# Performance work log

Measured on AMD Instinct MI355X. Metric: run time of the kernel, lower is better.

Reference implementation:

```python
import jax, jax.numpy as jnp
import numpy as np

D_MODEL = 1024
NUM_HEADS = 16
D_HEAD = D_MODEL // NUM_HEADS
EPS = 1e-06


def setup_inputs() -> dict:
    key = jax.random.key(0)
    ks = jax.random.split(key, 11)
    B, T = 16, 8192
    s = 1.0 / np.sqrt(D_MODEL)
    inp = {
        "query": jax.random.normal(ks[0], (B, 1, D_MODEL), jnp.float32),
        "key": jax.random.normal(ks[1], (B, T, D_MODEL), jnp.float32),
        "value": jax.random.normal(ks[2], (B, T, D_MODEL), jnp.float32),
        "Wq": jax.random.normal(ks[3], (D_MODEL, D_MODEL), jnp.float32) * s,
        "bq": jnp.zeros((D_MODEL,), jnp.float32),
        "Wk": jax.random.normal(ks[4], (D_MODEL, D_MODEL), jnp.float32) * s,
        "bk": jnp.zeros((D_MODEL,), jnp.float32),
        "Wv": jax.random.normal(ks[5], (D_MODEL, D_MODEL), jnp.float32) * s,
        "bv": jnp.zeros((D_MODEL,), jnp.float32),
        "Wo": jax.random.normal(ks[6], (D_MODEL, D_MODEL), jnp.float32) * s,
        "bo": jnp.zeros((D_MODEL,), jnp.float32),
    }
    return inp


def _feature_map(x):
    # ELU + 1 ensures positivity
    return jax.nn.elu(x) + 1.0


def reference(query, key, value, Wq, bq, Wk, bk, Wv, bv, Wo, bo):
    B, T, _ = key.shape
    H, dh = NUM_HEADS, D_HEAD
    # projections (torch Linear: x @ W^T + b)
    Q = (query @ Wq.T + bq).reshape(B, 1, H, dh).transpose(0, 2, 1, 3)  # [B,H,1,dh]
    K = (key @ Wk.T + bk).reshape(B, T, H, dh).transpose(0, 2, 1, 3)    # [B,H,T,dh]
    V = (value @ Wv.T + bv).reshape(B, T, H, dh).transpose(0, 2, 1, 3)  # [B,H,T,dh]
    Q = _feature_map(Q)
    K = _feature_map(K)
    # linear-attention accumulators
    KV = jnp.einsum("bhtd,bhte->bhde", K, V)        # [B,H,dh,dh]
    Z = K.sum(axis=2)                                  # [B,H,dh]
    num = jnp.einsum("bhqd,bhde->bhqe", Q, KV)       # [B,H,1,dh]
    den = jnp.einsum("bhqd,bhd->bhq", Q, Z)[..., None]  # [B,H,1,1]
    out = num / (den + EPS)
    out = out.transpose(0, 2, 1, 3).reshape(B, 1, D_MODEL)
    return out @ Wo.T + bo
```

## Files before the change

kernel.cpp:

```cpp
#include <hip/hip_runtime.h>


typedef __attribute__((ext_vector_type(8))) short  bf16x8;
typedef __attribute__((ext_vector_type(4))) short  bf16x4;
typedef __attribute__((ext_vector_type(4))) float  f32x4;

#define WS_QPHI 0u
#define WS_PRE  65536u
#define WS_S    131072u
#define WS_WKB  1179648u
#define WS_W    3276800u

__device__ __forceinline__ unsigned short f2bf(float f) {
  union { float f; unsigned u; } c; c.f = f;
  unsigned u = c.u;
  return (unsigned short)((u + 0x7fffu + ((u >> 16) & 1u)) >> 16);
}

__device__ __forceinline__ unsigned cvt_pk_bf16(float lo, float hi) {
  unsigned r;
  asm("v_cvt_pk_bf16_f32 %0, %1, %2" : "=v"(r) : "v"(lo), "v"(hi));
  return r;
}

__device__ __forceinline__ uint4 pack_bf16x8(f32x4 x, f32x4 y) {
  uint4 r;
  r.x = cvt_pk_bf16(x[0], x[1]); r.y = cvt_pk_bf16(x[2], x[3]);
  r.z = cvt_pk_bf16(y[0], y[1]); r.w = cvt_pk_bf16(y[2], y[3]);
  return r;
}

__device__ __forceinline__ void gload_lds16(const void* g, void* l) {
  __builtin_amdgcn_global_load_lds((const __attribute__((address_space(1))) void*)g,
                                   (__attribute__((address_space(3))) void*)l, 16, 0, 0);
}

__global__ void k_convert_wk(const float* __restrict__ Wk, unsigned short* __restrict__ Wkb) {
  int i = blockIdx.x * 256 + threadIdx.x;
  f32x4 v = ((const f32x4*)Wk)[i];
  bf16x4 o;
  o[0] = (short)f2bf(v[0]); o[1] = (short)f2bf(v[1]);
  o[2] = (short)f2bf(v[2]); o[3] = (short)f2bf(v[3]);
  ((bf16x4*)Wkb)[i] = o;
}

__global__ void k_qproj(const float* __restrict__ q, const float* __restrict__ Wq,
                        const float* __restrict__ bq, float* __restrict__ Qphi) {
  int b = blockIdx.x, h = blockIdx.y, d = threadIdx.x;
  const f32x4* qr = (const f32x4*)(q + b * 1024);
  const f32x4* wr = (const f32x4*)(Wq + (size_t)(h * 64 + d) * 1024);
  float s = bq[h * 64 + d];
  for (int i = 0; i < 256; ++i) {
    f32x4 a = qr[i], ww = wr[i];
    s += a[0]*ww[0] + a[1]*ww[1] + a[2]*ww[2] + a[3]*ww[3];
  }
  s = s > 0.f ? s + 1.f : __expf(s);
  Qphi[(b * 16 + h) * 64 + d] = s;
}

__global__ __launch_bounds__(512, 4)
void k_kproj(const float* __restrict__ key, const unsigned short* __restrict__ Wkb,
             const float* __restrict__ bk, const float* __restrict__ Qphi,
             float* __restrict__ w) {
  __shared__ __align__(16) unsigned short sA[2][128 * 40];
  __shared__ __align__(16) unsigned short sB[3][256 * 32];

  const int bid  = blockIdx.x + (blockIdx.y << 2);
  const int work = ((bid & 7) << 9) | (bid >> 3);
  const int np   = work & 3;
  const int mb   = work >> 2;
  const int b    = mb >> 6;
  const int mrow = (mb & 63) << 7;
  const int tid  = threadIdx.x;
  const int lane = tid & 63;
  const int wv   = tid >> 6;
  const int wr   = wv >> 2;
  const int wc   = wv & 3;
  const int n0   = np << 8;
  const int h    = (np << 2) | wc;
  const int l15  = lane & 15;
  const int lk   = (lane >> 4) << 3;

  const int ar = tid >> 2, aq = tid & 3;
  const float* Ab = key + ((size_t)((b << 13) + mrow + ar)) * 1024 + aq * 8;
  const int sAoff = ar * 40 + aq * 8;

  const int bsw = ((lane & 3) ^ ((lane >> 3) & 3)) << 3;
  const unsigned short* Bb = Wkb + ((size_t)(n0 + (wv << 5) + (lane >> 2))) * 1024 + bsw;
  const int fsw = (l15 >> 1) & 3;

  f32x4 acc[4][4];
  #pragma unroll
  for (int i = 0; i < 4; ++i)
    #pragma unroll
    for (int j = 0; j < 4; ++j) acc[i][j] = (f32x4)0.f;

  float qreg[4];
  #pragma unroll
  for (int ni = 0; ni < 4; ++ni)
    qreg[ni] = Qphi[((b << 4) + h) * 64 + ni * 16 + l15];

  f32x4 a0 = *(const f32x4*)(Ab);
  f32x4 a1 = *(const f32x4*)(Ab + 4);
  __builtin_amdgcn_sched_barrier(0);
  gload_lds16(Bb,                  &sB[0][wv * 1024]);
  gload_lds16(Bb + 16 * 1024,      &sB[0][wv * 1024 + 512]);
  gload_lds16(Bb + 32,             &sB[1][wv * 1024]);
  gload_lds16(Bb + 16 * 1024 + 32, &sB[1][wv * 1024 + 512]);
  __builtin_amdgcn_sched_barrier(0);
  *(uint4*)&sA[0][sAoff] = pack_bf16x8(a0, a1);
  asm volatile("s_waitcnt vmcnt(2) lgkmcnt(0)" ::: "memory");
  __builtin_amdgcn_s_barrier();
  __builtin_amdgcn_sched_barrier(0);

  #pragma unroll 1
  for (int t = 0; t < 32; ++t) {
    if (t < 31) {
      const float* An = Ab + (t + 1) * 32;
      a0 = *(const f32x4*)(An);
      a1 = *(const f32x4*)(An + 4);
    }
    __builtin_amdgcn_sched_barrier(0);
    if (t < 30) {
      const unsigned short* Bn = Bb + (t + 2) * 32;
      const int bn = (t + 2) % 3;
      gload_lds16(Bn,             &sB[bn][wv * 1024]);
      gload_lds16(Bn + 16 * 1024, &sB[bn][wv * 1024 + 512]);
    }
    __builtin_amdgcn_sched_barrier(0);
    {
      const unsigned short* pA = &sA[t & 1][0];
      const unsigned short* pB = &sB[t % 3][0];
      bf16x8 af[4], bfr[4];
      #pragma unroll
      for (int mi = 0; mi < 4; ++mi)
        af[mi] = *(const bf16x8*)&pA[((wr << 6) + mi * 16 + l15) * 40 + lk];
      #pragma unroll
      for (int ni = 0; ni < 4; ++ni)
        bfr[ni] = *(const bf16x8*)&pB[((wc << 6) + ni * 16 + l15) * 32
                                      + (((lane >> 4) ^ fsw) << 3)];
      #pragma unroll
      for (int mi = 0; mi < 4; ++mi)
        #pragma unroll
        for (int ni = 0; ni < 4; ++ni)
          acc[mi][ni] = __builtin_amdgcn_mfma_f32_16x16x32_bf16(af[mi], bfr[ni], acc[mi][ni], 0, 0, 0);
    }
    if (t < 31)
      *(uint4*)&sA[(t + 1) & 1][sAoff] = pack_bf16x8(a0, a1);
    if (t < 30)      asm volatile("s_waitcnt vmcnt(2) lgkmcnt(0)" ::: "memory");
    else if (t < 31) asm volatile("s_waitcnt vmcnt(0) lgkmcnt(0)" ::: "memory");
    if (t < 31) {
      __builtin_amdgcn_s_barrier();
      __builtin_amdgcn_sched_barrier(0);
    }
  }

  float bias[4];
  #pragma unroll
  for (int ni = 0; ni < 4; ++ni) bias[ni] = bk[n0 + (wc << 6) + ni * 16 + l15];

  #pragma unroll
  for (int mi = 0; mi < 4; ++mi) {
    float wa[4];
    #pragma unroll
    for (int r = 0; r < 4; ++r) {
      float s = 0.f;
      #pragma unroll
      for (int ni = 0; ni < 4; ++ni) {
        float x = acc[mi][ni][r] + bias[ni];
        x = x > 0.f ? x + 1.f : __expf(x);
        s += x * qreg[ni];
      }
      wa[r] = s;
    }
    #pragma unroll
    for (int m = 1; m < 16; m <<= 1)
      #pragma unroll
      for (int r = 0; r < 4; ++r) wa[r] += __shfl_xor(wa[r], m, 64);
    if (l15 == 0) {
      const int rg = lane >> 4;
      #pragma unroll
      for (int r = 0; r < 4; ++r) {
        int trow = mrow + (wr << 6) + mi * 16 + (rg << 2) + r;
        w[(((size_t)((b << 4) + h)) << 13) + trow] = wa[r];
      }
    }
  }
}

__global__ __launch_bounds__(256)
void k_sgemm(const float* __restrict__ value, const float* __restrict__ w,
             float* __restrict__ S) {
  __shared__ float wl[16 * 256];
  const int b = blockIdx.x, tc = blockIdx.y;
  const int t0 = tc << 8;
  const int tid = threadIdx.x;
  for (int i = tid; i < 16 * 256; i += 256)
    wl[i] = w[(((size_t)(b * 16 + (i >> 8))) << 13) + t0 + (i & 255)];
  __syncthreads();
  f32x4 acc[16];
  #pragma unroll
  for (int h = 0; h < 16; ++h) acc[h] = (f32x4)0.f;
  const f32x4* vb = (const f32x4*)(value + ((size_t)(b << 13) + t0) * 1024) + tid;
  #pragma unroll 4
  for (int t = 0; t < 256; ++t) {
    f32x4 x = vb[t << 8];
    #pragma unroll
    for (int h = 0; h < 16; ++h)
      acc[h] += x * wl[(h << 8) + t];
  }
  #pragma unroll
  for (int h = 0; h < 16; ++h) {
    float* sp = S + ((b << 4) + h) * 1024 + (tid << 2);
    atomicAdd(sp + 0, acc[h][0]); atomicAdd(sp + 1, acc[h][1]);
    atomicAdd(sp + 2, acc[h][2]); atomicAdd(sp + 3, acc[h][3]);
  }
}

__global__ __launch_bounds__(256)
void k_numden(const float* __restrict__ w, const float* __restrict__ S,
              const float* __restrict__ Wv, const float* __restrict__ bv,
              float* __restrict__ pre) {
  __shared__ float red[2][4][64];
  const int b = blockIdx.x, h = blockIdx.y;
  const int tid = threadIdx.x, e = tid & 63, part = tid >> 6;
  const float* wb = w + (((size_t)(b * 16 + h)) << 13);
  float dsum = 0.f;
  for (int i = part * 32; i < part * 32 + 32; ++i) dsum += wb[i * 64 + e];
  const f32x4* sr  = (const f32x4*)(S + (b * 16 + h) * 1024);
  const f32x4* wvr = (const f32x4*)(Wv + (size_t)(h * 64 + e) * 1024);
  float ns = 0.f;
  for (int i = part * 64; i < part * 64 + 64; ++i) {
    f32x4 a = sr[i], c = wvr[i];
    ns += a[0]*c[0] + a[1]*c[1] + a[2]*c[2] + a[3]*c[3];
  }
  red[0][part][e] = dsum; red[1][part][e] = ns;
  __syncthreads();
  if (part == 0) {
    float d = red[0][0][e] + red[0][1][e] + red[0][2][e] + red[0][3][e];
    float n = red[1][0][e] + red[1][1][e] + red[1][2][e] + red[1][3][e];
    #pragma unroll
    for (int m = 1; m < 64; m <<= 1) d += __shfl_xor(d, m, 64);
    n += d * bv[h * 64 + e];
    pre[b * 1024 + h * 64 + e] = n / (d + 1e-6f);
  }
}

__global__ __launch_bounds__(256)
void k_outproj(const float* __restrict__ pre, const float* __restrict__ Wo,
               const float* __restrict__ bo, float* __restrict__ out) {
  __shared__ float pl[1024];
  const int b = blockIdx.x, ch = blockIdx.y;
  const int tid = threadIdx.x, lane = tid & 63, wv = tid >> 6;
  for (int i = tid; i < 1024; i += 256) pl[i] = pre[b * 1024 + i];
  __syncthreads();
  for (int oi = 0; oi < 32; ++oi) {
    int o = (ch << 7) + (wv << 5) + oi;
    const f32x4* wrow = (const f32x4*)(Wo + (size_t)o * 1024);
    float s = 0.f;
    #pragma unroll
    for (int j = 0; j < 4; ++j) {
      f32x4 v = wrow[lane * 4 + j];
      f32x4 p = *(const f32x4*)&pl[(lane * 4 + j) * 4];
      s += v[0]*p[0] + v[1]*p[1] + v[2]*p[2] + v[3]*p[3];
    }
    #pragma unroll
    for (int m = 1; m < 64; m <<= 1) s += __shfl_xor(s, m, 64);
    if (lane == 0) out[b * 1024 + o] = s + bo[o];
  }
}

extern "C" void kernel_launch(void* const* d_in, const int* in_sizes, int n_in,
                              void* d_out, int out_size, void* d_ws, size_t ws_size,
                              hipStream_t stream) {
  const float* query = (const float*)d_in[0];
  const float* key   = (const float*)d_in[1];
  const float* value = (const float*)d_in[2];
  const float* Wq    = (const float*)d_in[3];
  const float* bq    = (const float*)d_in[4];
  const float* Wk    = (const float*)d_in[5];
  const float* bk    = (const float*)d_in[6];
  const float* Wv    = (const float*)d_in[7];
  const float* bv    = (const float*)d_in[8];
  const float* Wo    = (const float*)d_in[9];
  const float* bo    = (const float*)d_in[10];
  float* out = (float*)d_out;
  char* ws = (char*)d_ws;
  float*          Qphi = (float*)(ws + WS_QPHI);
  float*          pre  = (float*)(ws + WS_PRE);
  float*          S    = (float*)(ws + WS_S);
  unsigned short* Wkb  = (unsigned short*)(ws + WS_WKB);
  float*          w    = (float*)(ws + WS_W);

  hipMemsetAsync(S, 0, 16 * 16 * 1024 * sizeof(float), stream);
  k_convert_wk<<<1024, 256, 0, stream>>>(Wk, Wkb);
  k_qproj<<<dim3(16, 16), 64, 0, stream>>>(query, Wq, bq, Qphi);
  k_kproj<<<dim3(4, 1024), 512, 0, stream>>>(key, Wkb, bk, Qphi, w);
  k_sgemm<<<dim3(16, 32), 256, 0, stream>>>(value, w, S);
  k_numden<<<dim3(16, 16), 256, 0, stream>>>(w, S, Wv, bv, pre);
  k_outproj<<<dim3(16, 8), 256, 0, stream>>>(pre, Wo, bo, out);
}
```

Measured before the change: 653.1 us.

## Enlarge kproj GEMM tile to 256x256 with split-phase MFMA pipeline

The key-projection GEMM tile grows from 128x256 to 256x256 rows per block, with each wave now covering 128 rows in two halves. Each K step is split into two barrier-separated MFMA phases that use s_setprio, and the next B tile is loaded directly into LDS between the phases. A is prefetched two steps ahead in registers, and both A and B use an XOR-swizzled layout. The aim is to halve redundant reads of the key matrix and improve arithmetic intensity, at the cost of more registers (occupancy hint drops from 4 to 2) and more barriers per iteration.

Measured after the change: 771.4 us. 18.1% more time.

```diff
diff --git a/kernel.cpp b/kernel.cpp
--- a/kernel.cpp
+++ b/kernel.cpp
@@ -58,40 +58,44 @@
   Qphi[(b * 16 + h) * 64 + d] = s;
 }
 
-__global__ __launch_bounds__(512, 4)
+__global__ __launch_bounds__(512, 2)
 void k_kproj(const float* __restrict__ key, const unsigned short* __restrict__ Wkb,
              const float* __restrict__ bk, const float* __restrict__ Qphi,
              float* __restrict__ w) {
-  __shared__ __align__(16) unsigned short sA[2][128 * 40];
-  __shared__ __align__(16) unsigned short sB[3][256 * 32];
-
-  const int bid  = blockIdx.x + (blockIdx.y << 2);
-  const int work = ((bid & 7) << 9) | (bid >> 3);
+  __shared__ __align__(16) unsigned short sA[2][256 * 32];
+  __shared__ __align__(16) unsigned short sB[2][256 * 32];
+
+  const int bid  = blockIdx.x;
+  const int work = ((bid & 7) << 8) | (bid >> 3);
   const int np   = work & 3;
   const int mb   = work >> 2;
-  const int b    = mb >> 6;
-  const int mrow = (mb & 63) << 7;
+  const int row0 = mb << 8;
+  const int b    = mb >> 5;
+  const int n0   = np << 8;
   const int tid  = threadIdx.x;
   const int lane = tid & 63;
   const int wv   = tid >> 6;
   const int wr   = wv >> 2;
   const int wc   = wv & 3;
-  const int n0   = np << 8;
   const int h    = (np << 2) | wc;
   const int l15  = lane & 15;
-  const int lk   = (lane >> 4) << 3;
-
-  const int ar = tid >> 2, aq = tid & 3;
-  const float* Ab = key + ((size_t)((b << 13) + mrow + ar)) * 1024 + aq * 8;
-  const int sAoff = ar * 40 + aq * 8;
-
-  const int bsw = ((lane & 3) ^ ((lane >> 3) & 3)) << 3;
-  const unsigned short* Bb = Wkb + ((size_t)(n0 + (wv << 5) + (lane >> 2))) * 1024 + bsw;
-  const int fsw = (l15 >> 1) & 3;
-
-  f32x4 acc[4][4];
-  #pragma unroll
-  for (int i = 0; i < 4; ++i)
+  const int l16  = lane >> 4;
+
+  const int rdoff = l15 * 32 + ((l16 ^ ((l15 >> 1) & 3)) << 3);
+
+  const int ra = tid >> 1, ha = tid & 1;
+  const float* Ag = key + (size_t)(row0 + ra) * 1024 + ha * 16;
+  const int aw0 = ra * 32 + ((((ha << 1) | 0) ^ ((ra >> 1) & 3)) << 3);
+  const int aw1 = ra * 32 + ((((ha << 1) | 1) ^ ((ra >> 1) & 3)) << 3);
+
+  const int br  = tid >> 2;
+  const int bsw = ((tid & 3) ^ ((tid >> 3) & 3)) << 3;
+  const unsigned short* Bg0 = Wkb + (size_t)(n0 + br) * 1024 + bsw;
+  const unsigned short* Bg1 = Wkb + (size_t)(n0 + 128 + br) * 1024 + bsw;
+
+  f32x4 acc[8][4];
+  #pragma unroll
+  for (int i = 0; i < 8; ++i)
     #pragma unroll
     for (int j = 0; j < 4; ++j) acc[i][j] = (f32x4)0.f;
 
@@ -100,55 +104,76 @@
   for (int ni = 0; ni < 4; ++ni)
     qreg[ni] = Qphi[((b << 4) + h) * 64 + ni * 16 + l15];
 
-  f32x4 a0 = *(const f32x4*)(Ab);
-  f32x4 a1 = *(const f32x4*)(Ab + 4);
-  __builtin_amdgcn_sched_barrier(0);
-  gload_lds16(Bb,                  &sB[0][wv * 1024]);
-  gload_lds16(Bb + 16 * 1024,      &sB[0][wv * 1024 + 512]);
-  gload_lds16(Bb + 32,             &sB[1][wv * 1024]);
-  gload_lds16(Bb + 16 * 1024 + 32, &sB[1][wv * 1024 + 512]);
-  __builtin_amdgcn_sched_barrier(0);
-  *(uint4*)&sA[0][sAoff] = pack_bf16x8(a0, a1);
-  asm volatile("s_waitcnt vmcnt(2) lgkmcnt(0)" ::: "memory");
+  f32x4 ar[4];
+
+  #pragma unroll
+  for (int q = 0; q < 4; ++q) ar[q] = *(const f32x4*)(Ag + q * 4);
+  gload_lds16(Bg0,      &sB[0][wv * 512]);
+  gload_lds16(Bg1,      &sB[0][4096 + wv * 512]);
+  gload_lds16(Bg0 + 32, &sB[1][wv * 512]);
+  gload_lds16(Bg1 + 32, &sB[1][4096 + wv * 512]);
+  *(uint4*)&sA[0][aw0] = pack_bf16x8(ar[0], ar[1]);
+  *(uint4*)&sA[0][aw1] = pack_bf16x8(ar[2], ar[3]);
+  #pragma unroll
+  for (int q = 0; q < 4; ++q) ar[q] = *(const f32x4*)(Ag + 32 + q * 4);
+  asm volatile("s_waitcnt vmcnt(6) lgkmcnt(0)" ::: "memory");
   __builtin_amdgcn_s_barrier();
   __builtin_amdgcn_sched_barrier(0);
 
   #pragma unroll 1
   for (int t = 0; t < 32; ++t) {
+    const int s = t & 1;
+    const unsigned short* pA = &sA[s][0];
+    const unsigned short* pB = &sB[s][0];
     if (t < 31) {
-      const float* An = Ab + (t + 1) * 32;
-      a0 = *(const f32x4*)(An);
-      a1 = *(const f32x4*)(An + 4);
-    }
+      *(uint4*)&sA[s ^ 1][aw0] = pack_bf16x8(ar[0], ar[1]);
+      *(uint4*)&sA[s ^ 1][aw1] = pack_bf16x8(ar[2], ar[3]);
+    }
+    if (t < 30) {
+      const float* An = Ag + (t + 2) * 32;
+      #pragma unroll
+      for (int q = 0; q < 4; ++q) ar[q] = *(const f32x4*)(An + q * 4);
+    }
+    bf16x8 af[4], bfr[4];
+    #pragma unroll
+    for (int mi = 0; mi < 4; ++mi)
+      af[mi] = *(const bf16x8*)&pA[(wr * 128 + mi * 16) * 32 + rdoff];
+    #pragma unroll
+    for (int ni = 0; ni < 4; ++ni)
+      bfr[ni] = *(const bf16x8*)&pB[(wc * 64 + ni * 16) * 32 + rdoff];
+    __builtin_amdgcn_s_barrier();
+    asm volatile("s_waitcnt lgkmcnt(0)" ::: "memory");
+    __builtin_amdgcn_sched_barrier(0);
+    __builtin_amdgcn_s_setprio(1);
+    #pragma unroll
+    for (int mi = 0; mi < 4; ++mi)
+      #pragma unroll
+      for (int ni = 0; ni < 4; ++ni)
+        acc[mi][ni] = __builtin_amdgcn_mfma_f32_16x16x32_bf16(af[mi], bfr[ni], acc[mi][ni], 0, 0, 0);
+    __builtin_amdgcn_s_setprio(0);
+    __builtin_amdgcn_s_barrier();
     __builtin_amdgcn_sched_barrier(0);
     if (t < 30) {
-      const unsigned short* Bn = Bb + (t + 2) * 32;
-      const int bn = (t + 2) % 3;
-      gload_lds16(Bn,             &sB[bn][wv * 1024]);
-      gload_lds16(Bn + 16 * 1024, &sB[bn][wv * 1024 + 512]);
-    }
+      gload_lds16(Bg0 + (t + 2) * 32, &sB[s][wv * 512]);
+      gload_lds16(Bg1 + (t + 2) * 32, &sB[s][4096 + wv * 512]);
+    }
+    #pragma unroll
+    for (int mi = 0; mi < 4; ++mi)
+      af[mi] = *(const bf16x8*)&pA[((wr * 128 + 64) + mi * 16) * 32 + rdoff];
+    __builtin_amdgcn_s_barrier();
+    asm volatile("s_waitcnt lgkmcnt(0)" ::: "memory");
     __builtin_amdgcn_sched_barrier(0);
-    {
-      const unsigned short* pA = &sA[t & 1][0];
-      const unsigned short* pB = &sB[t % 3][0];
-      bf16x8 af[4], bfr[4];
-      #pragma unroll
-      for (int mi = 0; mi < 4; ++mi)
-        af[mi] = *(const bf16x8*)&pA[((wr << 6) + mi * 16 + l15) * 40 + lk];
+    __builtin_amdgcn_s_setprio(1);
+    #pragma unroll
+    for (int mi = 0; mi < 4; ++mi)
       #pragma unroll
       for (int ni = 0; ni < 4; ++ni)
-        bfr[ni] = *(const bf16x8*)&pB[((wc << 6) + ni * 16 + l15) * 32
-                                      + (((lane >> 4) ^ fsw) << 3)];
-      #pragma unroll
-      for (int mi = 0; mi < 4; ++mi)
-        #pragma unroll
-        for (int ni = 0; ni < 4; ++ni)
-          acc[mi][ni] = __builtin_amdgcn_mfma_f32_16x16x32_bf16(af[mi], bfr[ni], acc[mi][ni], 0, 0, 0);
-    }
-    if (t < 31)
-      *(uint4*)&sA[(t + 1) & 1][sAoff] = pack_bf16x8(a0, a1);
-    if (t < 30)      asm volatile("s_waitcnt vmcnt(2) lgkmcnt(0)" ::: "memory");
-    else if (t < 31) asm volatile("s_waitcnt vmcnt(0) lgkmcnt(0)" ::: "memory");
+        acc[4 + mi][ni] = __builtin_amdgcn_mfma_f32_16x16x32_bf16(af[mi], bfr[ni], acc[4 + mi][ni], 0, 0, 0);
+    __builtin_amdgcn_s_setprio(0);
+    __builtin_amdgcn_s_barrier();
+    __builtin_amdgcn_sched_barrier(0);
+    if (t < 30)      asm volatile("s_waitcnt vmcnt(6)" ::: "memory");
+    else if (t < 31) asm volatile("s_waitcnt vmcnt(0)" ::: "memory");
     if (t < 31) {
       __builtin_amdgcn_s_barrier();
       __builtin_amdgcn_sched_barrier(0);
@@ -158,9 +183,10 @@
   float bias[4];
   #pragma unroll
   for (int ni = 0; ni < 4; ++ni) bias[ni] = bk[n0 + (wc << 6) + ni * 16 + l15];
-
-  #pragma unroll
-  for (int mi = 0; mi < 4; ++mi) {
+  const int tbase = (mb & 31) << 8;
+
+  #pragma unroll
+  for (int mi = 0; mi < 8; ++mi) {
     float wa[4];
     #pragma unroll
     for (int r = 0; r < 4; ++r) {
@@ -178,10 +204,9 @@
       #pragma unroll
       for (int r = 0; r < 4; ++r) wa[r] += __shfl_xor(wa[r], m, 64);
     if (l15 == 0) {
-      const int rg = lane >> 4;
       #pragma unroll
       for (int r = 0; r < 4; ++r) {
-        int trow = mrow + (wr << 6) + mi * 16 + (rg << 2) + r;
+        int trow = tbase + (wr << 7) + mi * 16 + (l16 << 2) + r;
         w[(((size_t)((b << 4) + h)) << 13) + trow] = wa[r];
       }
     }
@@ -295,7 +320,7 @@
   hipMemsetAsync(S, 0, 16 * 16 * 1024 * sizeof(float), stream);
   k_convert_wk<<<1024, 256, 0, stream>>>(Wk, Wkb);
   k_qproj<<<dim3(16, 16), 64, 0, stream>>>(query, Wq, bq, Qphi);
-  k_kproj<<<dim3(4, 1024), 512, 0, stream>>>(key, Wkb, bk, Qphi, w);
+  k_kproj<<<2048, 512, 0, stream>>>(key, Wkb, bk, Qphi, w);
   k_sgemm<<<dim3(16, 32), 256, 0, stream>>>(value, w, S);
   k_numden<<<dim3(16, 16), 256, 0, stream>>>(w, S, Wv, bv, pre);
   k_outproj<<<dim3(16, 8), 256, 0, stream>>>(pre, Wo, bo, out);
```
